# Kernel optimization log

Hardware: AMD Instinct MI355X
Metric: run time of the kernel (lower is better)

The kernel has to match this reference:

```python
import math
import jax
import jax.numpy as jnp
import numpy as np

MUL = 32            # multiplicity of 0e and 1o in irreps_in/out
N_NODES = 50000
N_EDGES = 800000
N_BASIS = 10
N_HID = 100
NUM_NEIGHBORS = 16.0


def setup_inputs() -> dict:
    key = jax.random.key(0)
    ks = jax.random.split(key, 14)
    return {
        "node_input": jax.random.normal(ks[0], (N_NODES, 4 * MUL), jnp.float32),
        "node_attr": jnp.ones((N_NODES, 1), jnp.float32),
        "edge_src": jax.random.randint(ks[1], (N_EDGES,), 0, N_NODES, dtype=jnp.int32),
        "edge_dst": jax.random.randint(ks[2], (N_EDGES,), 0, N_NODES, dtype=jnp.int32),
        "edge_attr": jax.random.normal(ks[3], (N_EDGES, 4), jnp.float32),
        "edge_length_embedded": jax.random.uniform(ks[4], (N_EDGES, N_BASIS), dtype=jnp.float32),
        "W_sc0": jax.random.normal(ks[5], (MUL, MUL), jnp.float32),
        "W_sc1": jax.random.normal(ks[6], (MUL, MUL), jnp.float32),
        "W_l10": jax.random.normal(ks[7], (MUL, MUL), jnp.float32),
        "W_l11": jax.random.normal(ks[8], (MUL, MUL), jnp.float32),
        "W_l20": jax.random.normal(ks[9], (2 * MUL, MUL), jnp.float32),
        "W_l21": jax.random.normal(ks[10], (2 * MUL, MUL), jnp.float32),
        "W_fc1": jax.random.normal(ks[11], (N_BASIS, N_HID), jnp.float32),
        "W_fc2": jax.random.normal(ks[12], (N_HID, 4 * MUL), jnp.float32),
    }


def _fctp(x0, x1, attr, W0, W1):
    """FullyConnectedTensorProduct with a 1x0e attr: per-irrep linear * scalar attr.
    x0: [N,U], x1: [N,U,3], attr: [N,1]. Path norm alpha = 1/sqrt(fan_in)."""
    inv = 1.0 / math.sqrt(W0.shape[0])
    o0 = attr * (x0 @ W0) * inv                                    # [N,W]
    o1 = attr[:, :, None] * jnp.einsum("nud,uw->nwd", x1, W1) * inv  # [N,W,3]
    return o0, o1


def _forward(node_input, node_attr, edge_attr, edge_length_embedded,
             W_sc0, W_sc1, W_l10, W_l11, W_l20, W_l21, W_fc1, W_fc2,
             edge_src, edge_dst):
    N = node_input.shape[0]
    x0 = node_input[:, :MUL]                       # [N,32]  0e
    x1 = node_input[:, MUL:].reshape(N, MUL, 3)    # [N,32,3] 1o

    # self-connection and lin1 (both attr is scalar 0e)
    s0, s1 = _fctp(x0, x1, node_attr, W_sc0, W_sc1)
    y0, y1 = _fctp(x0, x1, node_attr, W_l10, W_l11)

    # radial MLP -> per-edge uvu weights (weight_numel = 4*MUL)
    h = jax.nn.silu(edge_length_embedded @ W_fc1 * (1.0 / math.sqrt(N_BASIS)))
    w = h @ W_fc2 * (1.0 / math.sqrt(N_HID))       # [E,128]
    w1, w2, w3, w4 = (w[:, 0*MUL:1*MUL], w[:, 1*MUL:2*MUL],
                      w[:, 2*MUL:3*MUL], w[:, 3*MUL:4*MUL])

    # gather source node features per edge
    x0s = y0[edge_src]                              # [E,32]
    x1s = y1[edge_src]                              # [E,32,3]
    ea0 = edge_attr[:, :1]                          # [E,1]   0e
    ea1 = edge_attr[:, 1:]                          # [E,3]   1o

    # segmented uvu tensor product (CG for lmax=1, component norm)
    mid0a = w1 * x0s * ea0                                         # 0e x 0e -> 0e
    mid0b = w4 * jnp.einsum("eum,em->eu", x1s, ea1) * (1.0 / math.sqrt(3.0))  # 1o x 1o -> 0e
    mid1a = (w2 * x0s)[:, :, None] * ea1[:, None, :]               # 0e x 1o -> 1o
    mid1b = w3[:, :, None] * x1s * ea0[:, None, :]                 # 1o x 0e -> 1o
    E = edge_attr.shape[0]
    edge_features = jnp.concatenate(
        [mid0a, mid0b, mid1a.reshape(E, -1), mid1b.reshape(E, -1)], axis=1)  # [E,256]

    # scatter-add to destination nodes
    agg = jax.ops.segment_sum(edge_features, edge_dst, num_segments=N)
    agg = agg * (1.0 / math.sqrt(NUM_NEIGHBORS))

    m0 = agg[:, :2 * MUL]                           # [N,64]  0e part of irreps_mid
    m1 = agg[:, 2 * MUL:].reshape(N, 2 * MUL, 3)    # [N,64,3] 1o part
    z0, z1 = _fctp(m0, m1, node_attr, W_l20, W_l21)

    # sc output_mask is all ones (every output irrep reachable)
    c_s = math.sin(math.pi / 8.0)
    c_x = math.cos(math.pi / 8.0)
    out0 = c_s * s0 + c_x * z0
    out1 = c_s * s1 + c_x * z1
    return jnp.concatenate([out0, out1.reshape(N, -1)], axis=1)   # [N,128]


def reference(node_input, node_attr, edge_src, edge_dst, edge_attr, edge_length_embedded,
              W_sc0, W_sc1, W_l10, W_l11, W_l20, W_l21, W_fc1, W_fc2):
    return _forward(node_input, node_attr, edge_attr, edge_length_embedded,
                    W_sc0, W_sc1, W_l10, W_l11, W_l20, W_l21, W_fc1, W_fc2,
                    edge_src, edge_dst)
```

## Files before the change

### kernel.cpp

```cpp
#include <hip/hip_runtime.h>
#include <hip/hip_bf16.h>

#define MUL 32
#define F4 128
#define NB 10
#define NH 100
#define EROW 136

#define INV_SQRT32 0.17677669529663687f
#define INV_SQRT10 0.31622776601683794f
#define INV_SQRT100 0.1f
#define INV_SQRT3 0.5773502691896258f
#define AGG_SCALE 0.25f
#define INV8 0.125f
#define C_S 0.3826834323650898f
#define C_X 0.9238795325112867f

typedef __attribute__((ext_vector_type(8))) short short8;
typedef __attribute__((ext_vector_type(4))) float float4v;

__device__ __forceinline__ float bf2f(__hip_bfloat16 v) { return __bfloat162float(v); }
__device__ __forceinline__ unsigned short f2b(float x) {
    __hip_bfloat16 b = __float2bfloat16(x);
    return *(unsigned short*)&b;
}
__device__ __forceinline__ float b2f(unsigned short u) {
    __hip_bfloat16 b;
    *(unsigned short*)&b = u;
    return __bfloat162float(b);
}
__device__ __forceinline__ float ldin(const void* p, size_t i, int f) {
    return f ? ((const float*)p)[i] : bf2f(((const __hip_bfloat16*)p)[i]);
}

__global__ void detect_dtype_kernel(const void* __restrict__ node_attr, int* __restrict__ flag) {
    unsigned w = *(const unsigned*)node_attr;
    *flag = (w == 0x3F800000u) ? 1 : 0;
}

__global__ __launch_bounds__(256) void prep_kernel(
    const void* __restrict__ Wfc1,
    const void* __restrict__ Wfc2,
    const void* __restrict__ Wl20,
    const void* __restrict__ Wl21,
    const int* __restrict__ flagp,
    unsigned short* __restrict__ w1t,
    unsigned short* __restrict__ w2t,
    unsigned short* __restrict__ w20t,
    unsigned short* __restrict__ w21t)
{
    int f = *flagp;
    int t = threadIdx.x;
    for (int i = t; i < 128 * 128; i += 256) {
        int n = i >> 7, k = i & 127;
        w2t[i] = (k < NH) ? f2b(ldin(Wfc2, (size_t)k * 128 + n, f)) : 0;
    }
    for (int i = t; i < 32 * 64; i += 256) {
        int v = i >> 6, u = i & 63;
        w20t[i] = f2b(ldin(Wl20, (size_t)u * 32 + v, f));
        w21t[i] = f2b(ldin(Wl21, (size_t)u * 32 + v, f));
    }
    for (int i = t; i < 112 * 32; i += 256) {
        int n = i >> 5, k = i & 31;
        w1t[i] = (k < NB && n < NH) ? f2b(ldin(Wfc1, (size_t)k * NH + n, f)) : 0;
    }
}

__global__ __launch_bounds__(256) void node_y_kernel(
    const void* __restrict__ node_input,
    const void* __restrict__ node_attr,
    const void* __restrict__ Wl10,
    const void* __restrict__ Wl11,
    const int* __restrict__ flagp,
    unsigned short* __restrict__ y, int N)
{
    __shared__ float sW0[1024];
    __shared__ float sW1[1024];
    __shared__ float sX[16 * 128];
    int f = *flagp;
    int t = threadIdx.x;
    for (int i = t; i < 1024; i += 256) {
        sW0[i] = ldin(Wl10, i, f);
        sW1[i] = ldin(Wl11, i, f);
    }
    int n0 = blockIdx.x * 16;
    for (int i = t; i < 2048; i += 256) {
        int ln = i >> 7, c = i & 127, n = n0 + ln;
        sX[i] = (n < N) ? ldin(node_input, (size_t)n * F4 + c, f) : 0.f;
    }
    __syncthreads();
    for (int i = t; i < 2048; i += 256) {
        int ln = i >> 7, c = i & 127, n = n0 + ln;
        if (n >= N) continue;
        float attr = ldin(node_attr, n, f);
        float acc = 0.f;
        if (c < 32) {
#pragma unroll
            for (int u = 0; u < 32; u++) acc += sX[ln * 128 + u] * sW0[u * 32 + c];
        } else {
            int d = (c - 32) >> 5, u0 = (c - 32) & 31;
#pragma unroll
            for (int u = 0; u < 32; u++) acc += sX[ln * 128 + 32 + u * 3 + d] * sW1[u * 32 + u0];
        }
        y[(size_t)n * F4 + c] = f2b(acc * attr * INV_SQRT32);
    }
}

#define SM_ELEB  0
#define SM_HW    4096
#define SM_Y     21504
#define SM_EA    38912
#define SM_SRC   39936
#define SM_DST   40192
#define SM_TOTAL 40448

__global__ __launch_bounds__(256, 4) void fused_edge_kernel(
    const void* __restrict__ ele,
    const void* __restrict__ eattr,
    const int* __restrict__ esrc,
    const int* __restrict__ edst,
    const int* __restrict__ flagp,
    const unsigned short* __restrict__ y,
    const unsigned short* __restrict__ w1t,
    const unsigned short* __restrict__ w2t,
    const unsigned short* __restrict__ w20t,
    const unsigned short* __restrict__ w21t,
    float* __restrict__ agg,
    int E)
{
    __shared__ __align__(16) char smem[SM_TOTAL];
    unsigned short* sEleB = (unsigned short*)(smem + SM_ELEB);
    unsigned short* sHW = (unsigned short*)(smem + SM_HW);
    unsigned short* sY = (unsigned short*)(smem + SM_Y);
    float* sEa = (float*)(smem + SM_EA);
    int* sSrc = (int*)(smem + SM_SRC);
    int* sDst = (int*)(smem + SM_DST);

    int f = *flagp;
    int t = threadIdx.x;
    int e0 = blockIdx.x * 64;
    int ne = E - e0;
    if (ne > 64) ne = 64;

    if (t < 64) {
        sSrc[t] = (t < ne) ? esrc[e0 + t] : 0;
        sDst[t] = (t < ne) ? edst[e0 + t] : 0;
    }
    for (int i = t; i < 64 * 32; i += 256) {
        int e = i >> 5, k = i & 31;
        float v = (k < NB && e < ne) ? ldin(ele, (size_t)(e0 + e) * NB + k, f) : 0.f;
        sEleB[i] = f2b(v);
    }
    {
        int e = t >> 2;
        sEa[t] = (e < ne) ? ldin(eattr, (size_t)e0 * 4 + t, f) : 0.f;
    }
    __syncthreads();

    int w = t >> 6, lane = t & 63;
    int lm = lane & 15, quad = lane >> 4;

    for (int i = t; i < 64 * 16; i += 256) {
        int e = i >> 4, q = i & 15;
        *(uint4*)(sY + e * EROW + q * 8) = *(const uint4*)(y + (size_t)sSrc[e] * 128 + q * 8);
    }

    {
        short8 a = *(const short8*)(sEleB + (w * 16 + lm) * 32 + quad * 8);
        float4v c1[7];
#pragma unroll
        for (int nt = 0; nt < 7; nt++) {
            c1[nt] = (float4v){0.f, 0.f, 0.f, 0.f};
            short8 b = *(const short8*)(w1t + (nt * 16 + lm) * 32 + quad * 8);
            c1[nt] = __builtin_amdgcn_mfma_f32_16x16x32_bf16(a, b, c1[nt], 0, 0, 0);
        }
#pragma unroll
        for (int nt = 0; nt < 7; nt++) {
            int ch = nt * 16 + lm;
#pragma unroll
            for (int r = 0; r < 4; r++) {
                int row = w * 16 + quad * 4 + r;
                float hv = 0.f;
                if (ch < NH) {
                    float aa = c1[nt][r] * INV_SQRT10;
                    hv = aa / (1.f + __expf(-aa));
                }
                sHW[row * EROW + ch] = f2b(hv);
            }
        }
        int e = t >> 2, seg = t & 3;
        *(uint2*)(sHW + e * EROW + 112 + seg * 4) = (uint2){0u, 0u};
    }
    __syncthreads();

    short8 a2[4];
#pragma unroll
    for (int kc = 0; kc < 4; kc++)
        a2[kc] = *(const short8*)(sHW + (w * 16 + lm) * EROW + kc * 32 + quad * 8);
    __syncthreads();
    {
        float4v c2[8];
#pragma unroll
        for (int nt = 0; nt < 8; nt++) c2[nt] = (float4v){0.f, 0.f, 0.f, 0.f};
#pragma unroll
        for (int kc = 0; kc < 4; kc++) {
#pragma unroll
            for (int nt = 0; nt < 8; nt++) {
                short8 b = *(const short8*)(w2t + (nt * 16 + lm) * 128 + kc * 32 + quad * 8);
                c2[nt] = __builtin_amdgcn_mfma_f32_16x16x32_bf16(a2[kc], b, c2[nt], 0, 0, 0);
            }
        }
#pragma unroll
        for (int nt = 0; nt < 8; nt++)
#pragma unroll
            for (int r = 0; r < 4; r++)
                sHW[(w * 16 + quad * 4 + r) * EROW + nt * 16 + lm] = f2b(c2[nt][r] * INV_SQRT100);
    }
    __syncthreads();

    {
        int em = w * 16 + lm;
        const unsigned short* wr = sHW + em * EROW;
        const unsigned short* yr = sY + em * EROW;
        short8 wA = *(const short8*)(wr + quad * 8);
        short8 wB = *(const short8*)(wr + 32 + quad * 8);
        short8 wC = *(const short8*)(wr + 64 + quad * 8);
        short8 wD = *(const short8*)(wr + 96 + quad * 8);
        short8 x0 = *(const short8*)(yr + quad * 8);
        short8 xd0 = *(const short8*)(yr + 32 + quad * 8);
        short8 xd1 = *(const short8*)(yr + 64 + quad * 8);
        short8 xd2 = *(const short8*)(yr + 96 + quad * 8);
        float ea0 = sEa[em * 4 + 0];
        float e1x = sEa[em * 4 + 1];
        float e1y = sEa[em * 4 + 2];
        float e1z = sEa[em * 4 + 3];
        float ea0S = ea0 * AGG_SCALE;
        float s3 = AGG_SCALE * INV_SQRT3;

        short8 f00, f01, f10, f11, f20, f21, f30, f31;
#pragma unroll
        for (int j = 0; j < 8; j++) {
            float x0f = b2f((unsigned short)x0[j]);
            float d0f = b2f((unsigned short)xd0[j]);
            float d1f = b2f((unsigned short)xd1[j]);
            float d2f = b2f((unsigned short)xd2[j]);
            f00[j] = (short)f2b(b2f((unsigned short)wA[j]) * x0f * ea0S);
            float tt = d0f * e1x + d1f * e1y + d2f * e1z;
            f01[j] = (short)f2b(b2f((unsigned short)wD[j]) * tt * s3);
            float p = b2f((unsigned short)wB[j]) * x0f * AGG_SCALE;
            f10[j] = (short)f2b(p * e1x);
            f20[j] = (short)f2b(p * e1y);
            f30[j] = (short)f2b(p * e1z);
            float q = b2f((unsigned short)wC[j]) * ea0S;
            f11[j] = (short)f2b(q * d0f);
            f21[j] = (short)f2b(q * d1f);
            f31[j] = (short)f2b(q * d2f);
        }

        float4v acc[8];
#pragma unroll
        for (int i = 0; i < 8; i++) acc[i] = (float4v){0.f, 0.f, 0.f, 0.f};
#pragma unroll
        for (int g = 0; g < 4; g++) {
            const unsigned short* wt = g ? w21t : w20t;
            short8 ak0 = (g == 0) ? f00 : (g == 1) ? f10 : (g == 2) ? f20 : f30;
            short8 ak1 = (g == 0) ? f01 : (g == 1) ? f11 : (g == 2) ? f21 : f31;
#pragma unroll
            for (int nt = 0; nt < 2; nt++) {
                short8 b0 = *(const short8*)(wt + (nt * 16 + lm) * 64 + quad * 8);
                short8 b1 = *(const short8*)(wt + (nt * 16 + lm) * 64 + 32 + quad * 8);
                acc[g * 2 + nt] = __builtin_amdgcn_mfma_f32_16x16x32_bf16(ak0, b0, acc[g * 2 + nt], 0, 0, 0);
                acc[g * 2 + nt] = __builtin_amdgcn_mfma_f32_16x16x32_bf16(ak1, b1, acc[g * 2 + nt], 0, 0, 0);
            }
        }
#pragma unroll
        for (int g = 0; g < 4; g++)
#pragma unroll
            for (int nt = 0; nt < 2; nt++)
#pragma unroll
                for (int r = 0; r < 4; r++) {
                    int er = w * 16 + quad * 4 + r;
                    if (er < ne) {
                        int ch = (g == 0) ? (nt * 16 + lm) : (32 + (g - 1) * 32 + nt * 16 + lm);
                        atomicAdd(&agg[(size_t)sDst[er] * F4 + ch], acc[g * 2 + nt][r]);
                    }
                }
    }
}

__global__ __launch_bounds__(256) void out_kernel(
    const void* __restrict__ node_input,
    const void* __restrict__ node_attr,
    const void* __restrict__ Wsc0,
    const void* __restrict__ Wsc1,
    const float* __restrict__ agg,
    const int* __restrict__ flagp,
    void* __restrict__ out, int N)
{
    __shared__ float sWs0[1024], sWs1[1024];
    __shared__ float sX[16 * 128];
    __shared__ float sA[16 * 128];
    int f = *flagp;
    int t = threadIdx.x;
    for (int i = t; i < 1024; i += 256) {
        sWs0[i] = ldin(Wsc0, i, f);
        sWs1[i] = ldin(Wsc1, i, f);
    }
    int n0 = blockIdx.x * 16;
    for (int i = t; i < 2048; i += 256) {
        int ln = i >> 7, c = i & 127, n = n0 + ln;
        sX[i] = (n < N) ? ldin(node_input, (size_t)n * F4 + c, f) : 0.f;
        sA[i] = (n < N) ? agg[(size_t)n * F4 + c] : 0.f;
    }
    __syncthreads();
    for (int i = t; i < 2048; i += 256) {
        int ln = i >> 7, c = i & 127, n = n0 + ln;
        if (n >= N) continue;
        float attr = ldin(node_attr, n, f);
        float s, z;
        if (c < 32) {
            float as = 0.f;
#pragma unroll
            for (int u = 0; u < 32; u++) as += sX[ln * 128 + u] * sWs0[u * 32 + c];
            s = as * INV_SQRT32;
            z = sA[ln * 128 + c];
        } else {
            int i2 = c - 32;
            int u0 = i2 / 3, d = i2 - u0 * 3;
            float as = 0.f;
#pragma unroll
            for (int u = 0; u < 32; u++) as += sX[ln * 128 + 32 + u * 3 + d] * sWs1[u * 32 + u0];
            s = as * INV_SQRT32;
            z = sA[ln * 128 + 32 + d * 32 + u0];
        }
        float val = attr * (C_S * s + C_X * z * INV8);
        size_t oi = (size_t)n * F4 + c;
        if (f) ((float*)out)[oi] = val;
        else   ((__hip_bfloat16*)out)[oi] = __float2bfloat16(val);
    }
}

extern "C" void kernel_launch(void* const* d_in, const int* in_sizes, int n_in,
                              void* d_out, int out_size, void* d_ws, size_t ws_size,
                              hipStream_t stream) {
    const void* node_input = d_in[0];
    const void* node_attr  = d_in[1];
    const int* edge_src    = (const int*)d_in[2];
    const int* edge_dst    = (const int*)d_in[3];
    const void* edge_attr  = d_in[4];
    const void* ele        = d_in[5];
    const void* Wsc0       = d_in[6];
    const void* Wsc1       = d_in[7];
    const void* Wl10       = d_in[8];
    const void* Wl11       = d_in[9];
    const void* Wl20       = d_in[10];
    const void* Wl21       = d_in[11];
    const void* Wfc1       = d_in[12];
    const void* Wfc2       = d_in[13];

    int N = in_sizes[0] / F4;
    int E = in_sizes[2];

    char* ws = (char*)d_ws;
    int* flag = (int*)ws;
    unsigned short* y = (unsigned short*)(ws + 64);
    size_t y_b = (size_t)N * F4 * 2;
    float* agg = (float*)(ws + 64 + y_b);
    size_t agg_b = (size_t)N * F4 * 4;
    size_t off = 64 + y_b + agg_b;
    unsigned short* w2t  = (unsigned short*)(ws + off);
    unsigned short* w20t = (unsigned short*)(ws + off + 32768);
    unsigned short* w21t = (unsigned short*)(ws + off + 36864);
    unsigned short* w1t  = (unsigned short*)(ws + off + 40960);

    detect_dtype_kernel<<<1, 1, 0, stream>>>(node_attr, flag);
    prep_kernel<<<1, 256, 0, stream>>>(Wfc1, Wfc2, Wl20, Wl21, flag, w1t, w2t, w20t, w21t);
    hipMemsetAsync(agg, 0, agg_b, stream);

    node_y_kernel<<<(N + 15) / 16, 256, 0, stream>>>(node_input, node_attr, Wl10, Wl11, flag, y, N);

    fused_edge_kernel<<<(E + 63) / 64, 256, 0, stream>>>(
        ele, edge_attr, edge_src, edge_dst, flag, y, w1t, w2t, w20t, w21t, agg, E);

    out_kernel<<<(N + 15) / 16, 256, 0, stream>>>(node_input, node_attr, Wsc0, Wsc1,
                                                  agg, flag, d_out, N);
}
```

Before: 665.7 us.

## Use packed fp16 atomics for scatter and load gathered rows directly to registers

The scatter-add accumulator changes from fp32 to fp16 and uses packed global_atomic_pk_add_f16, with lane-pair shuffles so each atomic writes two adjacent channels. This halves both the atomic count and the agg buffer traffic. The gathered y rows now go straight from global memory into registers instead of being staged in LDS, which shrinks shared memory and allows the occupancy hint to rise from 4 to 6. Accumulating about 16 edges per node in fp16 loses precision and risks tolerance failures.

```diff
diff --git a/kernel.cpp b/kernel.cpp
--- a/kernel.cpp
+++ b/kernel.cpp
@@ -1,5 +1,6 @@
 #include <hip/hip_runtime.h>
 #include <hip/hip_bf16.h>
+#include <hip/hip_fp16.h>
 
 #define MUL 32
 #define F4 128
@@ -31,6 +32,13 @@
 }
 __device__ __forceinline__ float ldin(const void* p, size_t i, int f) {
     return f ? ((const float*)p)[i] : bf2f(((const __hip_bfloat16*)p)[i]);
+}
+
+__device__ __forceinline__ void atomic_pk_add_f16(void* p, float lo, float hi) {
+    __half2 h = __floats2half2_rn(lo, hi);
+    unsigned int pk = *(unsigned int*)&h;
+    asm volatile("global_atomic_pk_add_f16 %0, %1, off"
+                 :: "v"((unsigned long long)p), "v"(pk) : "memory");
 }
 
 __global__ void detect_dtype_kernel(const void* __restrict__ node_attr, int* __restrict__ flag) {
@@ -108,13 +116,12 @@
 
 #define SM_ELEB  0
 #define SM_HW    4096
-#define SM_Y     21504
-#define SM_EA    38912
-#define SM_SRC   39936
-#define SM_DST   40192
-#define SM_TOTAL 40448
-
-__global__ __launch_bounds__(256, 4) void fused_edge_kernel(
+#define SM_EA    21504
+#define SM_SRC   22528
+#define SM_DST   22784
+#define SM_TOTAL 23040
+
+__global__ __launch_bounds__(256, 6) void fused_edge_kernel(
     const void* __restrict__ ele,
     const void* __restrict__ eattr,
     const int* __restrict__ esrc,
@@ -125,13 +132,12 @@
     const unsigned short* __restrict__ w2t,
     const unsigned short* __restrict__ w20t,
     const unsigned short* __restrict__ w21t,
-    float* __restrict__ agg,
+    __half* __restrict__ agg,
     int E)
 {
     __shared__ __align__(16) char smem[SM_TOTAL];
     unsigned short* sEleB = (unsigned short*)(smem + SM_ELEB);
     unsigned short* sHW = (unsigned short*)(smem + SM_HW);
-    unsigned short* sY = (unsigned short*)(smem + SM_Y);
     float* sEa = (float*)(smem + SM_EA);
     int* sSrc = (int*)(smem + SM_SRC);
     int* sDst = (int*)(smem + SM_DST);
@@ -159,11 +165,13 @@
 
     int w = t >> 6, lane = t & 63;
     int lm = lane & 15, quad = lane >> 4;
-
-    for (int i = t; i < 64 * 16; i += 256) {
-        int e = i >> 4, q = i & 15;
-        *(uint4*)(sY + e * EROW + q * 8) = *(const uint4*)(y + (size_t)sSrc[e] * 128 + q * 8);
-    }
+    int em = w * 16 + lm;
+
+    const unsigned short* yrg = y + (size_t)sSrc[em] * 128;
+    short8 x0  = *(const short8*)(yrg + quad * 8);
+    short8 xd0 = *(const short8*)(yrg + 32 + quad * 8);
+    short8 xd1 = *(const short8*)(yrg + 64 + quad * 8);
+    short8 xd2 = *(const short8*)(yrg + 96 + quad * 8);
 
     {
         short8 a = *(const short8*)(sEleB + (w * 16 + lm) * 32 + quad * 8);
@@ -219,17 +227,11 @@
     __syncthreads();
 
     {
-        int em = w * 16 + lm;
         const unsigned short* wr = sHW + em * EROW;
-        const unsigned short* yr = sY + em * EROW;
         short8 wA = *(const short8*)(wr + quad * 8);
         short8 wB = *(const short8*)(wr + 32 + quad * 8);
         short8 wC = *(const short8*)(wr + 64 + quad * 8);
         short8 wD = *(const short8*)(wr + 96 + quad * 8);
-        short8 x0 = *(const short8*)(yr + quad * 8);
-        short8 xd0 = *(const short8*)(yr + 32 + quad * 8);
-        short8 xd1 = *(const short8*)(yr + 64 + quad * 8);
-        short8 xd2 = *(const short8*)(yr + 96 + quad * 8);
         float ea0 = sEa[em * 4 + 0];
         float e1x = sEa[em * 4 + 1];
         float e1y = sEa[em * 4 + 2];
@@ -273,18 +275,30 @@
                 acc[g * 2 + nt] = __builtin_amdgcn_mfma_f32_16x16x32_bf16(ak1, b1, acc[g * 2 + nt], 0, 0, 0);
             }
         }
-#pragma unroll
-        for (int g = 0; g < 4; g++)
-#pragma unroll
-            for (int nt = 0; nt < 2; nt++)
-#pragma unroll
-                for (int r = 0; r < 4; r++) {
-                    int er = w * 16 + quad * 4 + r;
-                    if (er < ne) {
-                        int ch = (g == 0) ? (nt * 16 + lm) : (32 + (g - 1) * 32 + nt * 16 + lm);
-                        atomicAdd(&agg[(size_t)sDst[er] * F4 + ch], acc[g * 2 + nt][r]);
-                    }
-                }
+
+        bool oddl = (lm & 1);
+#pragma unroll
+        for (int i = 0; i < 8; i++) {
+            int g = i >> 1, nt = i & 1;
+            int chbase = (g == 0) ? (nt * 16) : (32 + (g - 1) * 32 + nt * 16);
+            float p0 = __shfl_xor(acc[i][0], 1);
+            float p1 = __shfl_xor(acc[i][1], 1);
+            float p2 = __shfl_xor(acc[i][2], 1);
+            float p3 = __shfl_xor(acc[i][3], 1);
+            float lo0 = oddl ? p2 : acc[i][0];
+            float hi0 = oddl ? acc[i][2] : p0;
+            float lo1 = oddl ? p3 : acc[i][1];
+            float hi1 = oddl ? acc[i][3] : p1;
+            int r0 = oddl ? 2 : 0;
+            int er0 = w * 16 + quad * 4 + r0;
+            int er1 = er0 + 1;
+            int pc = chbase + (lm & ~1);
+            if (er0 < ne)
+                atomic_pk_add_f16(agg + (size_t)sDst[er0] * F4 + pc, lo0, hi0);
+            if (er1 < ne)
+                atomic_pk_add_f16(agg + (size_t)sDst[er1] * F4 + pc, lo1, hi1);
+        }
+        asm volatile("s_waitcnt vmcnt(0)" ::: "memory");
     }
 }
 
@@ -293,7 +307,7 @@
     const void* __restrict__ node_attr,
     const void* __restrict__ Wsc0,
     const void* __restrict__ Wsc1,
-    const float* __restrict__ agg,
+    const __half* __restrict__ agg,
     const int* __restrict__ flagp,
     void* __restrict__ out, int N)
 {
@@ -310,7 +324,7 @@
     for (int i = t; i < 2048; i += 256) {
         int ln = i >> 7, c = i & 127, n = n0 + ln;
         sX[i] = (n < N) ? ldin(node_input, (size_t)n * F4 + c, f) : 0.f;
-        sA[i] = (n < N) ? agg[(size_t)n * F4 + c] : 0.f;
+        sA[i] = (n < N) ? __half2float(agg[(size_t)n * F4 + c]) : 0.f;
     }
     __syncthreads();
     for (int i = t; i < 2048; i += 256) {
@@ -365,8 +379,8 @@
     int* flag = (int*)ws;
     unsigned short* y = (unsigned short*)(ws + 64);
     size_t y_b = (size_t)N * F4 * 2;
-    float* agg = (float*)(ws + 64 + y_b);
-    size_t agg_b = (size_t)N * F4 * 4;
+    __half* agg = (__half*)(ws + 64 + y_b);
+    size_t agg_b = (size_t)N * F4 * 2;
     size_t off = 64 + y_b + agg_b;
     unsigned short* w2t  = (unsigned short*)(ws + off);
     unsigned short* w20t = (unsigned short*)(ws + off + 32768);
```

New measurement: 745.4 us. +12.0%, slower.

## Sort edges by destination and reduce runs in shared memory before atomics

Applied to the files above, without the earlier changes.

Adds a counting sort of edges by destination (histogram, single-block scan, scatter into a permutation), and the edge kernel now processes edges in sorted order. After the final MFMA stage, per-edge features go into shared memory as bf16. 128 threads then walk each channel and sum consecutive edges with the same destination, so there are far fewer global float atomics. The y rows are loaded straight from global into registers instead of being staged in LDS, which shrinks shared memory and raises the occupancy hint from 4 to 6. The cost is extra sort kernels (including a serial single-block scan over 50k nodes), gathered rather than coalesced edge-input reads, and an extra bf16 rounding of features before accumulation.

```diff
diff --git a/kernel.cpp b/kernel.cpp
--- a/kernel.cpp
+++ b/kernel.cpp
@@ -66,6 +66,55 @@
     }
 }
 
+__global__ __launch_bounds__(256) void hist_kernel(
+    const int* __restrict__ edst, int* __restrict__ cnt, int E)
+{
+    int i = blockIdx.x * 256 + threadIdx.x;
+    if (i < E) atomicAdd(&cnt[edst[i]], 1);
+}
+
+__global__ __launch_bounds__(1024) void scan_kernel(int* __restrict__ cnt, int N)
+{
+    __shared__ int wsum[16];
+    __shared__ int carry;
+    int t = threadIdx.x, lane = t & 63, wid = t >> 6;
+    if (t == 0) carry = 0;
+    __syncthreads();
+    for (int c0 = 0; c0 < N; c0 += 1024) {
+        int i = c0 + t;
+        int v = (i < N) ? cnt[i] : 0;
+        int x = v;
+#pragma unroll
+        for (int d = 1; d < 64; d <<= 1) { int y = __shfl_up(x, d); if (lane >= d) x += y; }
+        if (lane == 63) wsum[wid] = x;
+        __syncthreads();
+        if (wid == 0 && lane < 16) {
+            int s = wsum[lane];
+#pragma unroll
+            for (int d = 1; d < 16; d <<= 1) { int y = __shfl_up(s, d); if (lane >= d) s += y; }
+            wsum[lane] = s;
+        }
+        __syncthreads();
+        int pre = (wid > 0 ? wsum[wid - 1] : 0) + carry;
+        if (i < N) cnt[i] = pre + x - v;
+        int total = wsum[15] + carry;
+        __syncthreads();
+        if (t == 0) carry = total;
+        __syncthreads();
+    }
+}
+
+__global__ __launch_bounds__(256) void scatter_kernel(
+    const int* __restrict__ edst, int* __restrict__ cnt,
+    int* __restrict__ perm, int E)
+{
+    int i = blockIdx.x * 256 + threadIdx.x;
+    if (i < E) {
+        int p = atomicAdd(&cnt[edst[i]], 1);
+        perm[p] = i;
+    }
+}
+
 __global__ __launch_bounds__(256) void node_y_kernel(
     const void* __restrict__ node_input,
     const void* __restrict__ node_attr,
@@ -108,17 +157,18 @@
 
 #define SM_ELEB  0
 #define SM_HW    4096
-#define SM_Y     21504
-#define SM_EA    38912
-#define SM_SRC   39936
-#define SM_DST   40192
-#define SM_TOTAL 40448
-
-__global__ __launch_bounds__(256, 4) void fused_edge_kernel(
+#define SM_EA    21504
+#define SM_SRC   22528
+#define SM_DST   22784
+#define SM_PERM  23040
+#define SM_TOTAL 23296
+
+__global__ __launch_bounds__(256, 6) void fused_edge_kernel(
     const void* __restrict__ ele,
     const void* __restrict__ eattr,
     const int* __restrict__ esrc,
     const int* __restrict__ edst,
+    const int* __restrict__ perm,
     const int* __restrict__ flagp,
     const unsigned short* __restrict__ y,
     const unsigned short* __restrict__ w1t,
@@ -131,10 +181,10 @@
     __shared__ __align__(16) char smem[SM_TOTAL];
     unsigned short* sEleB = (unsigned short*)(smem + SM_ELEB);
     unsigned short* sHW = (unsigned short*)(smem + SM_HW);
-    unsigned short* sY = (unsigned short*)(smem + SM_Y);
     float* sEa = (float*)(smem + SM_EA);
     int* sSrc = (int*)(smem + SM_SRC);
     int* sDst = (int*)(smem + SM_DST);
+    int* sPerm = (int*)(smem + SM_PERM);
 
     int f = *flagp;
     int t = threadIdx.x;
@@ -142,28 +192,36 @@
     int ne = E - e0;
     if (ne > 64) ne = 64;
 
+    if (t < 64) sPerm[t] = (t < ne) ? perm[e0 + t] : -1;
+    __syncthreads();
+
     if (t < 64) {
-        sSrc[t] = (t < ne) ? esrc[e0 + t] : 0;
-        sDst[t] = (t < ne) ? edst[e0 + t] : 0;
+        int pe = sPerm[t];
+        sSrc[t] = (pe >= 0) ? esrc[pe] : 0;
+        sDst[t] = (pe >= 0) ? edst[pe] : -1;
     }
     for (int i = t; i < 64 * 32; i += 256) {
         int e = i >> 5, k = i & 31;
-        float v = (k < NB && e < ne) ? ldin(ele, (size_t)(e0 + e) * NB + k, f) : 0.f;
+        int pe = sPerm[e];
+        float v = (k < NB && pe >= 0) ? ldin(ele, (size_t)pe * NB + k, f) : 0.f;
         sEleB[i] = f2b(v);
     }
     {
         int e = t >> 2;
-        sEa[t] = (e < ne) ? ldin(eattr, (size_t)e0 * 4 + t, f) : 0.f;
+        int pe = sPerm[e];
+        sEa[t] = (pe >= 0) ? ldin(eattr, (size_t)pe * 4 + (t & 3), f) : 0.f;
     }
     __syncthreads();
 
     int w = t >> 6, lane = t & 63;
     int lm = lane & 15, quad = lane >> 4;
-
-    for (int i = t; i < 64 * 16; i += 256) {
-        int e = i >> 4, q = i & 15;
-        *(uint4*)(sY + e * EROW + q * 8) = *(const uint4*)(y + (size_t)sSrc[e] * 128 + q * 8);
-    }
+    int em = w * 16 + lm;
+
+    const unsigned short* yrg = y + (size_t)sSrc[em] * 128;
+    short8 x0  = *(const short8*)(yrg + quad * 8);
+    short8 xd0 = *(const short8*)(yrg + 32 + quad * 8);
+    short8 xd1 = *(const short8*)(yrg + 64 + quad * 8);
+    short8 xd2 = *(const short8*)(yrg + 96 + quad * 8);
 
     {
         short8 a = *(const short8*)(sEleB + (w * 16 + lm) * 32 + quad * 8);
@@ -219,17 +277,11 @@
     __syncthreads();
 
     {
-        int em = w * 16 + lm;
         const unsigned short* wr = sHW + em * EROW;
-        const unsigned short* yr = sY + em * EROW;
         short8 wA = *(const short8*)(wr + quad * 8);
         short8 wB = *(const short8*)(wr + 32 + quad * 8);
         short8 wC = *(const short8*)(wr + 64 + quad * 8);
         short8 wD = *(const short8*)(wr + 96 + quad * 8);
-        short8 x0 = *(const short8*)(yr + quad * 8);
-        short8 xd0 = *(const short8*)(yr + 32 + quad * 8);
-        short8 xd1 = *(const short8*)(yr + 64 + quad * 8);
-        short8 xd2 = *(const short8*)(yr + 96 + quad * 8);
         float ea0 = sEa[em * 4 + 0];
         float e1x = sEa[em * 4 + 1];
         float e1y = sEa[em * 4 + 2];
@@ -273,18 +325,37 @@
                 acc[g * 2 + nt] = __builtin_amdgcn_mfma_f32_16x16x32_bf16(ak1, b1, acc[g * 2 + nt], 0, 0, 0);
             }
         }
+
+        __syncthreads();
+        unsigned short* sFeat = (unsigned short*)smem;
 #pragma unroll
         for (int g = 0; g < 4; g++)
 #pragma unroll
-            for (int nt = 0; nt < 2; nt++)
+            for (int nt = 0; nt < 2; nt++) {
+                int ch = (g == 0) ? (nt * 16 + lm) : (32 + (g - 1) * 32 + nt * 16 + lm);
 #pragma unroll
                 for (int r = 0; r < 4; r++) {
                     int er = w * 16 + quad * 4 + r;
-                    if (er < ne) {
-                        int ch = (g == 0) ? (nt * 16 + lm) : (32 + (g - 1) * 32 + nt * 16 + lm);
-                        atomicAdd(&agg[(size_t)sDst[er] * F4 + ch], acc[g * 2 + nt][r]);
-                    }
+                    sFeat[er * EROW + ch] = f2b(acc[g * 2 + nt][r]);
                 }
+            }
+        __syncthreads();
+
+        if (t < 128) {
+            int c = t;
+            float s = 0.f;
+            int cur = -1;
+            for (int e = 0; e < 64; e++) {
+                int d = (e < ne) ? sDst[e] : -1;
+                if (d != cur) {
+                    if (cur >= 0) atomicAdd(&agg[(size_t)cur * F4 + c], s);
+                    s = 0.f;
+                    cur = d;
+                }
+                if (d >= 0) s += b2f(sFeat[e * EROW + c]);
+            }
+            if (cur >= 0) atomicAdd(&agg[(size_t)cur * F4 + c], s);
+        }
     }
 }
 
@@ -372,15 +443,24 @@
     unsigned short* w20t = (unsigned short*)(ws + off + 32768);
     unsigned short* w21t = (unsigned short*)(ws + off + 36864);
     unsigned short* w1t  = (unsigned short*)(ws + off + 40960);
+    size_t off2 = off + 49152;
+    int* cnt  = (int*)(ws + off2);
+    size_t cnt_b = ((size_t)N * 4 + 63) & ~(size_t)63;
+    int* perm = (int*)(ws + off2 + cnt_b);
 
     detect_dtype_kernel<<<1, 1, 0, stream>>>(node_attr, flag);
     prep_kernel<<<1, 256, 0, stream>>>(Wfc1, Wfc2, Wl20, Wl21, flag, w1t, w2t, w20t, w21t);
     hipMemsetAsync(agg, 0, agg_b, stream);
+    hipMemsetAsync(cnt, 0, (size_t)N * 4, stream);
+
+    hist_kernel<<<(E + 255) / 256, 256, 0, stream>>>(edge_dst, cnt, E);
+    scan_kernel<<<1, 1024, 0, stream>>>(cnt, N);
+    scatter_kernel<<<(E + 255) / 256, 256, 0, stream>>>(edge_dst, cnt, perm, E);
 
     node_y_kernel<<<(N + 15) / 16, 256, 0, stream>>>(node_input, node_attr, Wl10, Wl11, flag, y, N);
 
     fused_edge_kernel<<<(E + 63) / 64, 256, 0, stream>>>(
-        ele, edge_attr, edge_src, edge_dst, flag, y, w1t, w2t, w20t, w21t, agg, E);
+        ele, edge_attr, edge_src, edge_dst, perm, flag, y, w1t, w2t, w20t, w21t, agg, E);
 
     out_kernel<<<(N + 15) / 16, 256, 0, stream>>>(node_input, node_attr, Wsc0, Wsc1,
                                                   agg, flag, d_out, N);
```

Result: slower. 747.6 us (+12.3%).
